# Kernel optimization log

Hardware: AMD Instinct MI355X
Metric: run time of the kernel (lower is better)

Reference implementation:

```python
import jax, jax.numpy as jnp
import numpy as np

N = 50000        # num nodes
F = 64           # feature_size
G = 64           # graph_embedding_size
C = 4            # num_edge_cat
NNZ = 800000     # edges per category
L0 = 128         # first MLP hidden layer
EMB = 64         # embedding_size
EPS = 1e-5


def _glorot(key, shape):
    fan_in, fan_out = shape[-2], shape[-1]
    lim = jnp.sqrt(6.0 / (fan_in + fan_out))
    return jax.random.uniform(key, shape, jnp.float32, -lim, lim)


def setup_inputs() -> dict:
    key = jax.random.key(0)
    ks = jax.random.split(key, 8)
    A = jax.random.randint(ks[0], (C, 2, NNZ), 0, N, dtype=jnp.int64)
    X = jax.random.normal(ks[1], (N, F), jnp.float32)
    Ws = _glorot(ks[2], (C, F, G))            # per-edge-cat projection
    W0 = _glorot(ks[3], (C * G, L0))          # Linear0 weight (in,out)
    b0 = jnp.zeros((L0,), jnp.float32)
    gamma = jnp.ones((L0,), jnp.float32)      # BatchNorm1d weight
    beta = jnp.zeros((L0,), jnp.float32)      # BatchNorm1d bias
    W1 = _glorot(ks[4], (L0, EMB))            # Linear1 weight (in,out)
    b1 = jnp.zeros((EMB,), jnp.float32)
    return {"A": A, "X": X, "Ws": Ws, "W0": W0, "b0": b0,
            "gamma": gamma, "beta": beta, "W1": W1, "b1": b1,
            "mini_batch": 0}


def reference(A, X, Ws, W0, b0, gamma, beta, W1, b1, mini_batch):
    # mini_batch == False path. Instead of materializing dense NxN adjacency,
    # aggregate directly over edge lists (same math: (E @ X)[i] = sum_{(i,j) in E} X[j]).
    n = X.shape[0]
    XW = jnp.einsum('nf,cfg->cng', X, Ws)                       # [C,N,G]
    def agg(edges, xw):                                          # edges [2,nnz], xw [N,G]
        return jax.ops.segment_sum(xw[edges[1]], edges[0], num_segments=n)
    H = jax.vmap(agg)(A, XW)                                     # [C,N,G]
    H = jnp.transpose(H, (1, 0, 2)).reshape(n, -1)               # concat over edge cats -> [N, C*G]
    # NodeEmbedding: Linear -> BatchNorm1d (training stats) -> ELU -> Linear
    h = H @ W0 + b0
    mean = jnp.mean(h, axis=0)
    var = jnp.mean((h - mean) ** 2, axis=0)                      # biased var, as torch BN
    h = (h - mean) * jax.lax.rsqrt(var + EPS) * gamma + beta
    h = jax.nn.elu(h)
    return h @ W1 + b1                                           # [N, EMB]
```

## Files before the change

### kernel.cpp

```cpp
#include <hip/hip_runtime.h>
#include <hip/hip_bf16.h>

#define NN    50000
#define CC    4
#define NNZV  800000
#define TOTE  (CC * NNZV)
#define NWG   1024
#define EPW   (TOTE / NWG)
#define NBKT  256
#define RCAP  18432
#define CAPB  26624
#define NRB   782
#define NXB   782

using bf16 = __hip_bfloat16;
typedef short short8 __attribute__((ext_vector_type(8)));
typedef float f32x4  __attribute__((ext_vector_type(4)));
typedef unsigned short u16x8 __attribute__((ext_vector_type(8)));

__device__ __forceinline__ float bfu2f(unsigned short u) {
    union { unsigned int i; float f; } v;
    v.i = ((unsigned int)u) << 16;
    return v.f;
}
__device__ __forceinline__ float cvt(float x) { return x; }
__device__ __forceinline__ float cvt(bf16 x)  { return __bfloat162float(x); }
__device__ __forceinline__ unsigned short tobits(float x) {
    bf16 t = __float2bfloat16(x);
    return *(unsigned short*)&t;
}

__device__ __forceinline__ void detect_flags(const unsigned int* __restrict__ Xw,
                                             const unsigned int* __restrict__ Aw,
                                             int* dcnt, int& f32f, int& i64f) {
    const int t = threadIdx.x, nthr = blockDim.x;
    if (t < 2) dcnt[t] = 0;
    __syncthreads();
    int c1 = 0;
    for (int i = t; i < 1024; i += nthr) {
        unsigned b = (Xw[i] >> 7) & 0xFF;
        if (b >= 118 && b <= 134) c1++;
    }
    if (c1) atomicAdd(&dcnt[0], c1);
    if (t < 128) { if (Aw[2 * t + 1] == 0) atomicAdd(&dcnt[1], 1); }
    __syncthreads();
    f32f = (dcnt[0] < 512) ? 1 : 0;
    i64f = (dcnt[1] >= 96) ? 1 : 0;
    __syncthreads();
}

template<typename TF>
__device__ __forceinline__ void pack_body(const TF* __restrict__ W0, const TF* __restrict__ W1,
                                          const TF* __restrict__ Ws, const TF* __restrict__ b0,
                                          const TF* __restrict__ b1,
                                          unsigned short* __restrict__ Wb,
                                          unsigned short* __restrict__ Wb1,
                                          float* __restrict__ bias0, float* __restrict__ bias1,
                                          int trip) {
    const int lane = trip & 63;
    const int q = lane >> 4, cI = lane & 15;
    if (trip < 4096) {
        const int k0 = trip >> 9, t8 = (trip >> 6) & 7;
        const int kbase = k0 * 32 + q * 8;
        const int col   = t8 * 16 + cI;
        const int c     = kbase >> 6;
        float w0c[64];
        #pragma unroll
        for (int g = 0; g < 64; ++g)
            w0c[g] = cvt(W0[(size_t)(c * 64 + g) * 128 + col]);
        #pragma unroll
        for (int j = 0; j < 8; ++j) {
            const int f = (kbase + j) & 63;
            const TF* wsrow = Ws + ((size_t)c * 64 + f) * 64;
            float acc = 0.f;
            #pragma unroll
            for (int g = 0; g < 64; ++g)
                acc += cvt(wsrow[g]) * w0c[g];
            Wb[(size_t)trip * 8 + j] = tobits(acc);
        }
    } else if (trip < 5120) {
        const int u = trip - 4096;
        const int k0 = u >> 8, t4 = (u >> 6) & 3;
        #pragma unroll
        for (int j = 0; j < 8; ++j)
            Wb1[(size_t)u * 8 + j] =
                tobits(cvt(W1[(size_t)(k0 * 32 + q * 8 + j) * 64 + t4 * 16 + cI]));
    } else if (trip < 5248) {
        bias0[trip - 5120] = cvt(b0[trip - 5120]);
    } else if (trip < 5312) {
        bias1[trip - 5248] = cvt(b1[trip - 5248]);
    }
}

__global__ __launch_bounds__(256) void pack_kernel(const void* X, const void* A,
                                                   const void* W0, const void* W1,
                                                   const void* Ws, const void* b0,
                                                   const void* b1,
                                                   unsigned short* Wb, unsigned short* Wb1,
                                                   float* bias0, float* bias1,
                                                   unsigned int* zero512) {
    __shared__ int dcnt[2];
    int f32f, i64f;
    detect_flags((const unsigned int*)X, (const unsigned int*)A, dcnt, f32f, i64f);
    const int t = threadIdx.x;
    if (blockIdx.x == 0) { zero512[t] = 0u; zero512[t + 256] = 0u; }
    const int trip = blockIdx.x * 256 + t;
    if (trip >= 5312) return;
    if (f32f) pack_body<float>((const float*)W0, (const float*)W1, (const float*)Ws,
                               (const float*)b0, (const float*)b1, Wb, Wb1, bias0, bias1, trip);
    else      pack_body<bf16> ((const bf16*)W0, (const bf16*)W1, (const bf16*)Ws,
                               (const bf16*)b0, (const bf16*)b1, Wb, Wb1, bias0, bias1, trip);
}

template<typename TI>
__device__ __forceinline__ void cscat2_body(const TI* __restrict__ A,
                                            unsigned int* __restrict__ gcur,
                                            unsigned int* __restrict__ recs,
                                            unsigned int* lh, unsigned int* lrec) {
    const int w = blockIdx.x, t = threadIdx.x;
    lh[t] = 0;
    __syncthreads();
    const int base = w * EPW;
    for (int i = t; i < EPW; i += 256) {
        const int e  = base + i;
        const int c  = e / NNZV;
        const int ei = e - c * NNZV;
        const int dst = (int)A[(size_t)(c * 2 + 0) * NNZV + ei];
        const int src = (int)A[(size_t)(c * 2 + 1) * NNZV + ei];
        unsigned int rec = 0xFFFFFFFFu;
        if ((unsigned)dst < NN && (unsigned)src < NN) {
            rec = ((unsigned)dst << 16) | (unsigned)src;
            atomicAdd(&lh[dst >> 8], 1u);
        }
        lrec[i] = rec;
    }
    __syncthreads();
    const unsigned int myslice = atomicAdd(&gcur[t], lh[t]);
    __syncthreads();
    lh[t] = myslice;
    __syncthreads();
    for (int i = t; i < EPW; i += 256) {
        const unsigned int rec = lrec[i];
        if (rec == 0xFFFFFFFFu) continue;
        const int e   = base + i;
        const int c   = e / NNZV;
        const int dst = (int)(rec >> 16);
        const int src = (int)(rec & 0xFFFFu);
        const int b   = dst >> 8;
        const unsigned int pos = atomicAdd(&lh[b], 1u);
        if (pos < RCAP)
            recs[(size_t)b * RCAP + pos] =
                ((unsigned)(dst & 255) << 18) | ((unsigned)c << 16) | (unsigned)src;
    }
}

__device__ __forceinline__ void xconv_body(const void* __restrict__ X, int f32f,
                                           unsigned short* __restrict__ Xb, int bidx) {
    const size_t base = (size_t)bidx * 4096 + (size_t)threadIdx.x * 16;
    #pragma unroll
    for (int i = 0; i < 4; ++i) {
        const size_t off = base + (size_t)i * 4;
        if (off < (size_t)NN * 64) {
            ushort4 o;
            if (f32f) {
                const float4 v = *(const float4*)((const float*)X + off);
                o.x = tobits(v.x); o.y = tobits(v.y); o.z = tobits(v.z); o.w = tobits(v.w);
            } else {
                o = *(const ushort4*)((const unsigned short*)X + off);
            }
            *(ushort4*)(Xb + off) = o;
        } else if (off < (size_t)(NN + 1) * 64) {
            *(ushort4*)(Xb + off) = make_ushort4(0, 0, 0, 0);
        }
    }
}

__global__ __launch_bounds__(256) void fused_kernel(const void* __restrict__ X,
                                                    const void* __restrict__ A,
                                                    unsigned short* __restrict__ Xb,
                                                    unsigned int* __restrict__ gcur,
                                                    unsigned int* __restrict__ recs) {
    __shared__ unsigned int Su[256 + EPW];
    __shared__ int dcnt[2];
    int f32f, i64f;
    detect_flags((const unsigned int*)X, (const unsigned int*)A, dcnt, f32f, i64f);
    if (blockIdx.x < NWG) {
        unsigned int* lh   = Su;
        unsigned int* lrec = Su + 256;
        if (i64f) cscat2_body<long long>((const long long*)A, gcur, recs, lh, lrec);
        else      cscat2_body<int>      ((const int*)A,       gcur, recs, lh, lrec);
    } else {
        xconv_body(X, f32f, Xb, blockIdx.x - NWG);
    }
}

__global__ __launch_bounds__(1024) void dfinal_kernel(const unsigned int* __restrict__ gcur,
                                                      const unsigned int* __restrict__ recs,
                                                      unsigned short* __restrict__ edge_src,
                                                      int2* __restrict__ segd) {
    __shared__ unsigned int lrec[RCAP];
    __shared__ unsigned int scnt[1024], soff[1024], send[1024];
    __shared__ unsigned int ts[256];
    const int b = blockIdx.x, t = threadIdx.x;
    const size_t obase = (size_t)b * CAPB;
    int n = (int)gcur[b];
    if (n > RCAP) n = RCAP;
    const size_t rbase = (size_t)b * RCAP;
    scnt[t] = 0;
    __syncthreads();
    for (int i = t; i < n; i += 1024) {
        const unsigned int r = recs[rbase + i];
        lrec[i] = r;
        const int seg = (int)(((r >> 18) & 255u) * 4u + ((r >> 16) & 3u));
        atomicAdd(&scnt[seg], 1u);
    }
    __syncthreads();
    unsigned int v0 = 0, v1 = 0, v2 = 0, v3 = 0;
    unsigned int p0 = 0, p1 = 0, p2 = 0, p3 = 0, s = 0;
    if (t < 256) {
        const int j0 = t * 4;
        v0 = scnt[j0]; v1 = scnt[j0 + 1]; v2 = scnt[j0 + 2]; v3 = scnt[j0 + 3];
        p0 = (v0 + 7u) & ~7u; p1 = (v1 + 7u) & ~7u;
        p2 = (v2 + 7u) & ~7u; p3 = (v3 + 7u) & ~7u;
        s = p0 + p1 + p2 + p3;
        ts[t] = s;
    }
    __syncthreads();
    for (int off = 1; off < 256; off <<= 1) {
        unsigned int val = 0;
        if (t < 256 && t >= off) val = ts[t - off];
        __syncthreads();
        if (t < 256) ts[t] += val;
        __syncthreads();
    }
    if (t < 256) {
        const int j0 = t * 4;
        unsigned int ex = ts[t] - s;
        soff[j0]     = ex;
        send[j0]     = ex + p0;
        soff[j0 + 1] = ex + p0;
        send[j0 + 1] = ex + p0 + p1;
        soff[j0 + 2] = ex + p0 + p1;
        send[j0 + 2] = ex + p0 + p1 + p2;
        soff[j0 + 3] = ex + p0 + p1 + p2;
        send[j0 + 3] = ex + s;
    }
    __syncthreads();
    {
        const int dst = b * 256 + (t >> 2);
        if (dst < NN) {
            int2 o; o.x = (int)(obase + soff[t]); o.y = (int)scnt[t];
            segd[b * 1024 + t] = o;
        }
    }
    __syncthreads();
    for (int i = t; i < n; i += 1024) {
        const unsigned int r = lrec[i];
        const int seg = (int)(((r >> 18) & 255u) * 4u + ((r >> 16) & 3u));
        const unsigned int pos = atomicAdd(&soff[seg], 1u);
        edge_src[obase + pos] = (unsigned short)(r & 0xFFFFu);
    }
    __syncthreads();
    {
        unsigned int j = soff[t];
        const unsigned int e = send[t];
        for (; j < e; ++j) edge_src[obase + j] = (unsigned short)NN;
    }
}

__global__ __launch_bounds__(256) void gather_kernel(const unsigned short* __restrict__ edge_src,
                                                     const int2* __restrict__ segd,
                                                     const unsigned short* __restrict__ Xb,
                                                     unsigned short* __restrict__ S) {
    const int t   = threadIdx.x;
    const int gid = t >> 4;
    const int li  = t & 15;
    const int g4  = li * 4;
    const int dst = blockIdx.x * 4 + (gid >> 2);
    const int c   = gid & 3;
    const int2 sd = segd[dst * 4 + c];
    const int cnt  = sd.y;
    const int pcnt = (cnt + 7) & ~7;
    const unsigned short* ep = edge_src + sd.x;
    f32x4 acc = (f32x4){0.f, 0.f, 0.f, 0.f};
    if (pcnt > 0) {
        u16x8 idx = *(const u16x8*)(ep);
        for (int e0 = 0; e0 < pcnt; e0 += 8) {
            const u16x8 nidx = *(const u16x8*)(ep + e0 + 8);
            ushort4 v0 = *(const ushort4*)(Xb + (size_t)idx[0] * 64 + g4);
            ushort4 v1 = *(const ushort4*)(Xb + (size_t)idx[1] * 64 + g4);
            ushort4 v2 = *(const ushort4*)(Xb + (size_t)idx[2] * 64 + g4);
            ushort4 v3 = *(const ushort4*)(Xb + (size_t)idx[3] * 64 + g4);
            ushort4 v4 = *(const ushort4*)(Xb + (size_t)idx[4] * 64 + g4);
            ushort4 v5 = *(const ushort4*)(Xb + (size_t)idx[5] * 64 + g4);
            ushort4 v6 = *(const ushort4*)(Xb + (size_t)idx[6] * 64 + g4);
            ushort4 v7 = *(const ushort4*)(Xb + (size_t)idx[7] * 64 + g4);
            acc[0] += bfu2f(v0.x); acc[1] += bfu2f(v0.y); acc[2] += bfu2f(v0.z); acc[3] += bfu2f(v0.w);
            acc[0] += bfu2f(v1.x); acc[1] += bfu2f(v1.y); acc[2] += bfu2f(v1.z); acc[3] += bfu2f(v1.w);
            acc[0] += bfu2f(v2.x); acc[1] += bfu2f(v2.y); acc[2] += bfu2f(v2.z); acc[3] += bfu2f(v2.w);
            acc[0] += bfu2f(v3.x); acc[1] += bfu2f(v3.y); acc[2] += bfu2f(v3.z); acc[3] += bfu2f(v3.w);
            acc[0] += bfu2f(v4.x); acc[1] += bfu2f(v4.y); acc[2] += bfu2f(v4.z); acc[3] += bfu2f(v4.w);
            acc[0] += bfu2f(v5.x); acc[1] += bfu2f(v5.y); acc[2] += bfu2f(v5.z); acc[3] += bfu2f(v5.w);
            acc[0] += bfu2f(v6.x); acc[1] += bfu2f(v6.y); acc[2] += bfu2f(v6.z); acc[3] += bfu2f(v6.w);
            acc[0] += bfu2f(v7.x); acc[1] += bfu2f(v7.y); acc[2] += bfu2f(v7.z); acc[3] += bfu2f(v7.w);
            idx = nidx;
        }
    }
    ushort4 o;
    o.x = tobits(acc[0]); o.y = tobits(acc[1]); o.z = tobits(acc[2]); o.w = tobits(acc[3]);
    *(ushort4*)(S + (size_t)dst * 256 + c * 64 + g4) = o;
}

__global__ __launch_bounds__(256) void l0_mfma(const unsigned short* __restrict__ Hg,
                                               const unsigned short* __restrict__ Wb,
                                               const float* __restrict__ bias0,
                                               unsigned short* __restrict__ hO,
                                               float* __restrict__ stats) {
    __shared__ unsigned short Hs[64 * 264];
    __shared__ float psum[128], psq[128];
    const int t = threadIdx.x;
    const int n0 = blockIdx.x * 64;
    #pragma unroll
    for (int i = 0; i < 16; ++i) {
        const int r = (t >> 6) + i * 4;
        const int k = (t & 63) * 4;
        const int row = n0 + r;
        ushort4 v = make_ushort4(0, 0, 0, 0);
        if (row < NN) v = *(const ushort4*)(Hg + (size_t)row * 256 + k);
        *(ushort4*)(&Hs[r * 264 + k]) = v;
    }
    if (t < 128) { psum[t] = 0.f; psq[t] = 0.f; }
    __syncthreads();
    const int w = t >> 6, lane = t & 63;
    const int q = lane >> 4, cI = lane & 15;
    f32x4 acc[8];
    #pragma unroll
    for (int i = 0; i < 8; ++i) acc[i] = (f32x4){0.f, 0.f, 0.f, 0.f};
    const unsigned short* arow = &Hs[(w * 16 + cI) * 264 + q * 8];
    #pragma unroll
    for (int k0 = 0; k0 < 8; ++k0) {
        short8 a = *(const short8*)(arow + k0 * 32);
        #pragma unroll
        for (int t8 = 0; t8 < 8; ++t8) {
            short8 b = *(const short8*)(Wb + ((size_t)(k0 * 8 + t8) * 64 + lane) * 8);
            acc[t8] = __builtin_amdgcn_mfma_f32_16x16x32_bf16(a, b, acc[t8], 0, 0, 0);
        }
    }
    __syncthreads();
    const int rloc  = w * 16 + q * 4;
    const int rbase = n0 + rloc;
    #pragma unroll
    for (int t8 = 0; t8 < 8; ++t8) {
        const int col = t8 * 16 + cI;
        const float bc = bias0[col];
        float s = 0.f, qq = 0.f;
        #pragma unroll
        for (int r = 0; r < 4; ++r) {
            float v = acc[t8][r] + bc;
            Hs[(rloc + r) * 136 + col] = tobits(v);
            if (rbase + r >= NN) v = 0.f;
            s += v; qq += v * v;
        }
        s  += __shfl_xor(s, 16, 64);  s  += __shfl_xor(s, 32, 64);
        qq += __shfl_xor(qq, 16, 64); qq += __shfl_xor(qq, 32, 64);
        if (q == 0) { atomicAdd(&psum[col], s); atomicAdd(&psq[col], qq); }
    }
    __syncthreads();
    if (t < 128) { atomicAdd(&stats[t], psum[t]); atomicAdd(&stats[128 + t], psq[t]); }
    #pragma unroll
    for (int i = 0; i < 4; ++i) {
        const int m    = t + i * 256;
        const int row  = m >> 4;
        const int col0 = (m & 15) * 8;
        const int grow = n0 + row;
        if (grow < NN) {
            *(ushort4*)(hO + (size_t)grow * 128 + col0)     = *(ushort4*)(&Hs[row * 136 + col0]);
            *(ushort4*)(hO + (size_t)grow * 128 + col0 + 4) = *(ushort4*)(&Hs[row * 136 + col0 + 4]);
        }
    }
}

__global__ __launch_bounds__(256) void l1_mfma(const void* __restrict__ X,
                                               const void* __restrict__ A,
                                               const unsigned short* __restrict__ hg,
                                               const float* __restrict__ stats,
                                               const void* __restrict__ gamma,
                                               const void* __restrict__ beta,
                                               const unsigned short* __restrict__ Wb1,
                                               const float* __restrict__ bias1,
                                               void* __restrict__ outv) {
    __shared__ unsigned short Es[64 * 136];
    __shared__ float coefL[256];
    __shared__ int dcnt[2];
    int f32f, i64f;
    detect_flags((const unsigned int*)X, (const unsigned int*)A, dcnt, f32f, i64f);
    const int t = threadIdx.x;
    if (t < 128) {
        const float invN = 1.0f / (float)NN;
        const float mean = stats[t] * invN;
        const float var  = stats[128 + t] * invN - mean * mean;
        const float inv  = rsqrtf(var + 1e-5f);
        const float ga = f32f ? ((const float*)gamma)[t] : cvt(((const bf16*)gamma)[t]);
        const float be = f32f ? ((const float*)beta)[t]  : cvt(((const bf16*)beta)[t]);
        const float a = ga * inv;
        coefL[t] = a;
        coefL[128 + t] = be - mean * a;
    }
    __syncthreads();
    const int n0 = blockIdx.x * 64;
    #pragma unroll
    for (int i = 0; i < 8; ++i) {
        const int r = (t >> 5) + i * 8;
        const int k = (t & 31) * 4;
        const int row = n0 + r;
        ushort4 o = make_ushort4(0, 0, 0, 0);
        if (row < NN) {
            ushort4 v = *(const ushort4*)(hg + (size_t)row * 128 + k);
            float f0 = coefL[k + 0] * bfu2f(v.x) + coefL[128 + k + 0];
            float f1 = coefL[k + 1] * bfu2f(v.y) + coefL[128 + k + 1];
            float f2 = coefL[k + 2] * bfu2f(v.z) + coefL[128 + k + 2];
            float f3 = coefL[k + 3] * bfu2f(v.w) + coefL[128 + k + 3];
            f0 = f0 > 0.f ? f0 : expm1f(f0);
            f1 = f1 > 0.f ? f1 : expm1f(f1);
            f2 = f2 > 0.f ? f2 : expm1f(f2);
            f3 = f3 > 0.f ? f3 : expm1f(f3);
            o.x = tobits(f0); o.y = tobits(f1); o.z = tobits(f2); o.w = tobits(f3);
        }
        *(ushort4*)(&Es[r * 136 + k]) = o;
    }
    __syncthreads();
    const int w = t >> 6, lane = t & 63;
    const int q = lane >> 4, cI = lane & 15;
    f32x4 acc[4];
    #pragma unroll
    for (int i = 0; i < 4; ++i) acc[i] = (f32x4){0.f, 0.f, 0.f, 0.f};
    const unsigned short* arow = &Es[(w * 16 + cI) * 136 + q * 8];
    #pragma unroll
    for (int k0 = 0; k0 < 4; ++k0) {
        short8 a = *(const short8*)(arow + k0 * 32);
        #pragma unroll
        for (int t4 = 0; t4 < 4; ++t4) {
            short8 b = *(const short8*)(Wb1 + ((size_t)(k0 * 4 + t4) * 64 + lane) * 8);
            acc[t4] = __builtin_amdgcn_mfma_f32_16x16x32_bf16(a, b, acc[t4], 0, 0, 0);
        }
    }
    __syncthreads();
    float* ot = (float*)Es;
    const int rloc = w * 16 + q * 4;
    #pragma unroll
    for (int t4 = 0; t4 < 4; ++t4) {
        const int col = t4 * 16 + cI;
        const float bc = bias1[col];
        #pragma unroll
        for (int r = 0; r < 4; ++r)
            ot[(rloc + r) * 68 + col] = acc[t4][r] + bc;
    }
    __syncthreads();
    #pragma unroll
    for (int i = 0; i < 4; ++i) {
        const int m    = t + i * 256;
        const int row  = m >> 4;
        const int col0 = (m & 15) * 4;
        const int grow = n0 + row;
        if (grow >= NN) continue;
        const float f0 = ot[row * 68 + col0 + 0];
        const float f1 = ot[row * 68 + col0 + 1];
        const float f2 = ot[row * 68 + col0 + 2];
        const float f3 = ot[row * 68 + col0 + 3];
        if (f32f) {
            float4 o; o.x = f0; o.y = f1; o.z = f2; o.w = f3;
            *(float4*)((float*)outv + (size_t)grow * 64 + col0) = o;
        } else {
            ushort4 o;
            o.x = tobits(f0); o.y = tobits(f1); o.z = tobits(f2); o.w = tobits(f3);
            *(ushort4*)((unsigned short*)outv + (size_t)grow * 64 + col0) = o;
        }
    }
}

extern "C" void kernel_launch(void* const* d_in, const int* in_sizes, int n_in,
                              void* d_out, int out_size, void* d_ws, size_t ws_size,
                              hipStream_t stream) {
    const void* A     = d_in[0];
    const void* X     = d_in[1];
    const void* Ws    = d_in[2];
    const void* W0    = d_in[3];
    const void* b0    = d_in[4];
    const void* gamma = d_in[5];
    const void* beta  = d_in[6];
    const void* W1    = d_in[7];
    const void* b1    = d_in[8];

    char* ws = (char*)d_ws;
    unsigned short* Xb       = (unsigned short*)(ws);
    unsigned short* S        = (unsigned short*)(ws + 6400256);
    unsigned short* h        = (unsigned short*)(ws + 32000256);
    unsigned int*   recs     = (unsigned int*)  (ws + 44800256);
    int2*           segd     = (int2*)          (ws + 59250944);
    unsigned short* edge_src = (unsigned short*)(ws + 60850944);
    float*          stats    = (float*)         (ws + 71287552);
    unsigned int*   gcur     = (unsigned int*)  (ws + 71288576);
    unsigned short* Wb       = (unsigned short*)(ws + 71289600);
    unsigned short* Wb1      = (unsigned short*)(ws + 71355136);
    float*          bias0    = (float*)         (ws + 71371520);
    float*          bias1    = (float*)         (ws + 71372032);

    pack_kernel  <<<21, 256, 0, stream>>>(X, A, W0, W1, Ws, b0, b1,
                                          Wb, Wb1, bias0, bias1,
                                          (unsigned int*)stats );
    fused_kernel <<<NWG + NXB, 256, 0, stream>>>(X, A, Xb, gcur, recs);
    dfinal_kernel<<<196, 1024, 0, stream>>>(gcur, recs, edge_src, segd);
    gather_kernel<<<12500, 256, 0, stream>>>(edge_src, segd, Xb, S);
    l0_mfma      <<<NRB, 256, 0, stream>>>(S, Wb, bias0, h, stats);
    l1_mfma      <<<NRB, 256, 0, stream>>>(X, A, h, stats, gamma, beta, Wb1, bias1, d_out);
}
```

Baseline: 258.8 us.

## Fuse destination sort and gather into one kernel with finer 64-node buckets

Edges are now bucketed into 64-node destination buckets, split across 8 partitions to spread global atomics, instead of 256-node buckets. The separate finalize and gather kernels are merged into one kernel per bucket that sorts edges into a shared-memory list and immediately gathers and sums X rows. This removes the global edge_src/segd round trip and one launch. In exchange it adds per-partition capacity limits (768 records per partition per bucket) that could overflow and drop edges on skewed inputs, and it launches far fewer gather blocks, which may lower latency hiding.

```diff
diff --git a/kernel.cpp b/kernel.cpp
--- a/kernel.cpp
+++ b/kernel.cpp
@@ -7,9 +7,10 @@
 #define TOTE  (CC * NNZV)
 #define NWG   1024
 #define EPW   (TOTE / NWG)
-#define NBKT  256
-#define RCAP  18432
-#define CAPB  26624
+#define NFB   782
+#define NPART 8
+#define RCAPV 768
+#define BCAP  (NPART * RCAPV)
 #define NRB   782
 #define NXB   782
 
@@ -98,12 +99,14 @@
                                                    const void* b1,
                                                    unsigned short* Wb, unsigned short* Wb1,
                                                    float* bias0, float* bias1,
-                                                   unsigned int* zero512) {
+                                                   unsigned int* zeroReg) {
     __shared__ int dcnt[2];
     int f32f, i64f;
     detect_flags((const unsigned int*)X, (const unsigned int*)A, dcnt, f32f, i64f);
     const int t = threadIdx.x;
-    if (blockIdx.x == 0) { zero512[t] = 0u; zero512[t + 256] = 0u; }
+    if (blockIdx.x == 0) {
+        for (int i = t; i < 8448; i += 256) zeroReg[i] = 0u;
+    }
     const int trip = blockIdx.x * 256 + t;
     if (trip >= 5312) return;
     if (f32f) pack_body<float>((const float*)W0, (const float*)W1, (const float*)Ws,
@@ -118,39 +121,46 @@
                                             unsigned int* __restrict__ recs,
                                             unsigned int* lh, unsigned int* lrec) {
     const int w = blockIdx.x, t = threadIdx.x;
-    lh[t] = 0;
-    __syncthreads();
-    const int base = w * EPW;
+    const int v = w & (NPART - 1);
+    #pragma unroll
+    for (int u = 0; u < 4; ++u) lh[t + u * 256] = 0;
+    __syncthreads();
+    const int base   = w * EPW;
+    const int c      = base / NNZV;
+    const int eibase = base - c * NNZV;
+    const TI* Ad = A + (size_t)(c * 2 + 0) * NNZV + eibase;
+    const TI* As = A + (size_t)(c * 2 + 1) * NNZV + eibase;
     for (int i = t; i < EPW; i += 256) {
-        const int e  = base + i;
-        const int c  = e / NNZV;
-        const int ei = e - c * NNZV;
-        const int dst = (int)A[(size_t)(c * 2 + 0) * NNZV + ei];
-        const int src = (int)A[(size_t)(c * 2 + 1) * NNZV + ei];
+        const int dst = (int)Ad[i];
+        const int src = (int)As[i];
         unsigned int rec = 0xFFFFFFFFu;
         if ((unsigned)dst < NN && (unsigned)src < NN) {
             rec = ((unsigned)dst << 16) | (unsigned)src;
-            atomicAdd(&lh[dst >> 8], 1u);
+            atomicAdd(&lh[dst >> 6], 1u);
         }
         lrec[i] = rec;
     }
     __syncthreads();
-    const unsigned int myslice = atomicAdd(&gcur[t], lh[t]);
-    __syncthreads();
-    lh[t] = myslice;
-    __syncthreads();
+    unsigned int cl[4], sl[4];
+    #pragma unroll
+    for (int u = 0; u < 4; ++u) cl[u] = lh[t + u * 256];
+    __syncthreads();
+    #pragma unroll
+    for (int u = 0; u < 4; ++u)
+        sl[u] = cl[u] ? atomicAdd(&gcur[(v << 10) + t + u * 256], cl[u]) : 0u;
+    #pragma unroll
+    for (int u = 0; u < 4; ++u) lh[t + u * 256] = sl[u];
+    __syncthreads();
+    const unsigned int cb = (unsigned)c << 16;
     for (int i = t; i < EPW; i += 256) {
         const unsigned int rec = lrec[i];
         if (rec == 0xFFFFFFFFu) continue;
-        const int e   = base + i;
-        const int c   = e / NNZV;
         const int dst = (int)(rec >> 16);
-        const int src = (int)(rec & 0xFFFFu);
-        const int b   = dst >> 8;
+        const int b   = dst >> 6;
         const unsigned int pos = atomicAdd(&lh[b], 1u);
-        if (pos < RCAP)
-            recs[(size_t)b * RCAP + pos] =
-                ((unsigned)(dst & 255) << 18) | ((unsigned)c << 16) | (unsigned)src;
+        if (pos < RCAPV)
+            recs[((size_t)b * NPART + v) * RCAPV + pos] =
+                ((unsigned)(dst & 63) << 18) | cb | (rec & 0xFFFFu);
     }
 }
 
@@ -180,13 +190,13 @@
                                                     unsigned short* __restrict__ Xb,
                                                     unsigned int* __restrict__ gcur,
                                                     unsigned int* __restrict__ recs) {
-    __shared__ unsigned int Su[256 + EPW];
+    __shared__ unsigned int Su[1024 + EPW];
     __shared__ int dcnt[2];
     int f32f, i64f;
     detect_flags((const unsigned int*)X, (const unsigned int*)A, dcnt, f32f, i64f);
     if (blockIdx.x < NWG) {
         unsigned int* lh   = Su;
-        unsigned int* lrec = Su + 256;
+        unsigned int* lrec = Su + 1024;
         if (i64f) cscat2_body<long long>((const long long*)A, gcur, recs, lh, lrec);
         else      cscat2_body<int>      ((const int*)A,       gcur, recs, lh, lrec);
     } else {
@@ -194,37 +204,30 @@
     }
 }
 
-__global__ __launch_bounds__(1024) void dfinal_kernel(const unsigned int* __restrict__ gcur,
+__global__ __launch_bounds__(512) void dgather_kernel(const unsigned int* __restrict__ gcur,
                                                       const unsigned int* __restrict__ recs,
-                                                      unsigned short* __restrict__ edge_src,
-                                                      int2* __restrict__ segd) {
-    __shared__ unsigned int lrec[RCAP];
-    __shared__ unsigned int scnt[1024], soff[1024], send[1024];
-    __shared__ unsigned int ts[256];
+                                                      const unsigned short* __restrict__ Xb,
+                                                      unsigned short* __restrict__ S) {
+    __shared__ unsigned short elist[8192];
+    __shared__ unsigned int scnt[256], sstart[256], scur[256], send[256], ts[256];
+    __shared__ unsigned int cntv[NPART];
     const int b = blockIdx.x, t = threadIdx.x;
-    const size_t obase = (size_t)b * CAPB;
-    int n = (int)gcur[b];
-    if (n > RCAP) n = RCAP;
-    const size_t rbase = (size_t)b * RCAP;
-    scnt[t] = 0;
-    __syncthreads();
-    for (int i = t; i < n; i += 1024) {
-        const unsigned int r = recs[rbase + i];
-        lrec[i] = r;
-        const int seg = (int)(((r >> 18) & 255u) * 4u + ((r >> 16) & 3u));
-        atomicAdd(&scnt[seg], 1u);
-    }
-    __syncthreads();
-    unsigned int v0 = 0, v1 = 0, v2 = 0, v3 = 0;
-    unsigned int p0 = 0, p1 = 0, p2 = 0, p3 = 0, s = 0;
-    if (t < 256) {
-        const int j0 = t * 4;
-        v0 = scnt[j0]; v1 = scnt[j0 + 1]; v2 = scnt[j0 + 2]; v3 = scnt[j0 + 3];
-        p0 = (v0 + 7u) & ~7u; p1 = (v1 + 7u) & ~7u;
-        p2 = (v2 + 7u) & ~7u; p3 = (v3 + 7u) & ~7u;
-        s = p0 + p1 + p2 + p3;
-        ts[t] = s;
-    }
+    if (t < NPART) {
+        unsigned int n = gcur[(t << 10) + b];
+        cntv[t] = n < RCAPV ? n : RCAPV;
+    }
+    if (t < 256) scnt[t] = 0;
+    __syncthreads();
+    const size_t rb = (size_t)b * BCAP;
+    #pragma unroll
+    for (int v = 0; v < NPART; ++v) {
+        const int n = (int)cntv[v];
+        for (int i = t; i < n; i += 512)
+            atomicAdd(&scnt[recs[rb + v * RCAPV + i] >> 16], 1u);
+    }
+    __syncthreads();
+    unsigned int myp = 0;
+    if (t < 256) { myp = (scnt[t] + 7u) & ~7u; ts[t] = myp; }
     __syncthreads();
     for (int off = 1; off < 256; off <<= 1) {
         unsigned int val = 0;
@@ -234,81 +237,62 @@
         __syncthreads();
     }
     if (t < 256) {
-        const int j0 = t * 4;
-        unsigned int ex = ts[t] - s;
-        soff[j0]     = ex;
-        send[j0]     = ex + p0;
-        soff[j0 + 1] = ex + p0;
-        send[j0 + 1] = ex + p0 + p1;
-        soff[j0 + 2] = ex + p0 + p1;
-        send[j0 + 2] = ex + p0 + p1 + p2;
-        soff[j0 + 3] = ex + p0 + p1 + p2;
-        send[j0 + 3] = ex + s;
-    }
-    __syncthreads();
-    {
-        const int dst = b * 256 + (t >> 2);
+        const unsigned int ex = ts[t] - myp;
+        sstart[t] = ex; scur[t] = ex; send[t] = ex + myp;
+        for (unsigned int j = ex + scnt[t]; j < ex + myp; ++j)
+            elist[j] = (unsigned short)NN;
+    }
+    __syncthreads();
+    #pragma unroll
+    for (int v = 0; v < NPART; ++v) {
+        const int n = (int)cntv[v];
+        for (int i = t; i < n; i += 512) {
+            const unsigned int r = recs[rb + v * RCAPV + i];
+            const unsigned int pos = atomicAdd(&scur[r >> 16], 1u);
+            elist[pos] = (unsigned short)(r & 0xFFFFu);
+        }
+    }
+    __syncthreads();
+    const int g  = t >> 4;
+    const int li = t & 15;
+    const int g4 = li * 4;
+    #pragma unroll
+    for (int s8 = 0; s8 < 8; ++s8) {
+        const int seg = g * 8 + s8;
+        const int dst = b * 64 + (seg >> 2);
+        const int c   = seg & 3;
+        const int start = (int)sstart[seg];
+        const int pcnt  = (int)(send[seg] - sstart[seg]);
+        f32x4 acc = (f32x4){0.f, 0.f, 0.f, 0.f};
+        if (pcnt > 0) {
+            u16x8 idx = *(const u16x8*)(elist + start);
+            for (int e0 = 0; e0 < pcnt; e0 += 8) {
+                const u16x8 nidx = *(const u16x8*)(elist + start + e0 + 8);
+                ushort4 v0 = *(const ushort4*)(Xb + (size_t)idx[0] * 64 + g4);
+                ushort4 v1 = *(const ushort4*)(Xb + (size_t)idx[1] * 64 + g4);
+                ushort4 v2 = *(const ushort4*)(Xb + (size_t)idx[2] * 64 + g4);
+                ushort4 v3 = *(const ushort4*)(Xb + (size_t)idx[3] * 64 + g4);
+                ushort4 v4 = *(const ushort4*)(Xb + (size_t)idx[4] * 64 + g4);
+                ushort4 v5 = *(const ushort4*)(Xb + (size_t)idx[5] * 64 + g4);
+                ushort4 v6 = *(const ushort4*)(Xb + (size_t)idx[6] * 64 + g4);
+                ushort4 v7 = *(const ushort4*)(Xb + (size_t)idx[7] * 64 + g4);
+                acc[0] += bfu2f(v0.x); acc[1] += bfu2f(v0.y); acc[2] += bfu2f(v0.z); acc[3] += bfu2f(v0.w);
+                acc[0] += bfu2f(v1.x); acc[1] += bfu2f(v1.y); acc[2] += bfu2f(v1.z); acc[3] += bfu2f(v1.w);
+                acc[0] += bfu2f(v2.x); acc[1] += bfu2f(v2.y); acc[2] += bfu2f(v2.z); acc[3] += bfu2f(v2.w);
+                acc[0] += bfu2f(v3.x); acc[1] += bfu2f(v3.y); acc[2] += bfu2f(v3.z); acc[3] += bfu2f(v3.w);
+                acc[0] += bfu2f(v4.x); acc[1] += bfu2f(v4.y); acc[2] += bfu2f(v4.z); acc[3] += bfu2f(v4.w);
+                acc[0] += bfu2f(v5.x); acc[1] += bfu2f(v5.y); acc[2] += bfu2f(v5.z); acc[3] += bfu2f(v5.w);
+                acc[0] += bfu2f(v6.x); acc[1] += bfu2f(v6.y); acc[2] += bfu2f(v6.z); acc[3] += bfu2f(v6.w);
+                acc[0] += bfu2f(v7.x); acc[1] += bfu2f(v7.y); acc[2] += bfu2f(v7.z); acc[3] += bfu2f(v7.w);
+                idx = nidx;
+            }
+        }
         if (dst < NN) {
-            int2 o; o.x = (int)(obase + soff[t]); o.y = (int)scnt[t];
-            segd[b * 1024 + t] = o;
-        }
-    }
-    __syncthreads();
-    for (int i = t; i < n; i += 1024) {
-        const unsigned int r = lrec[i];
-        const int seg = (int)(((r >> 18) & 255u) * 4u + ((r >> 16) & 3u));
-        const unsigned int pos = atomicAdd(&soff[seg], 1u);
-        edge_src[obase + pos] = (unsigned short)(r & 0xFFFFu);
-    }
-    __syncthreads();
-    {
-        unsigned int j = soff[t];
-        const unsigned int e = send[t];
-        for (; j < e; ++j) edge_src[obase + j] = (unsigned short)NN;
-    }
-}
-
-__global__ __launch_bounds__(256) void gather_kernel(const unsigned short* __restrict__ edge_src,
-                                                     const int2* __restrict__ segd,
-                                                     const unsigned short* __restrict__ Xb,
-                                                     unsigned short* __restrict__ S) {
-    const int t   = threadIdx.x;
-    const int gid = t >> 4;
-    const int li  = t & 15;
-    const int g4  = li * 4;
-    const int dst = blockIdx.x * 4 + (gid >> 2);
-    const int c   = gid & 3;
-    const int2 sd = segd[dst * 4 + c];
-    const int cnt  = sd.y;
-    const int pcnt = (cnt + 7) & ~7;
-    const unsigned short* ep = edge_src + sd.x;
-    f32x4 acc = (f32x4){0.f, 0.f, 0.f, 0.f};
-    if (pcnt > 0) {
-        u16x8 idx = *(const u16x8*)(ep);
-        for (int e0 = 0; e0 < pcnt; e0 += 8) {
-            const u16x8 nidx = *(const u16x8*)(ep + e0 + 8);
-            ushort4 v0 = *(const ushort4*)(Xb + (size_t)idx[0] * 64 + g4);
-            ushort4 v1 = *(const ushort4*)(Xb + (size_t)idx[1] * 64 + g4);
-            ushort4 v2 = *(const ushort4*)(Xb + (size_t)idx[2] * 64 + g4);
-            ushort4 v3 = *(const ushort4*)(Xb + (size_t)idx[3] * 64 + g4);
-            ushort4 v4 = *(const ushort4*)(Xb + (size_t)idx[4] * 64 + g4);
-            ushort4 v5 = *(const ushort4*)(Xb + (size_t)idx[5] * 64 + g4);
-            ushort4 v6 = *(const ushort4*)(Xb + (size_t)idx[6] * 64 + g4);
-            ushort4 v7 = *(const ushort4*)(Xb + (size_t)idx[7] * 64 + g4);
-            acc[0] += bfu2f(v0.x); acc[1] += bfu2f(v0.y); acc[2] += bfu2f(v0.z); acc[3] += bfu2f(v0.w);
-            acc[0] += bfu2f(v1.x); acc[1] += bfu2f(v1.y); acc[2] += bfu2f(v1.z); acc[3] += bfu2f(v1.w);
-            acc[0] += bfu2f(v2.x); acc[1] += bfu2f(v2.y); acc[2] += bfu2f(v2.z); acc[3] += bfu2f(v2.w);
-            acc[0] += bfu2f(v3.x); acc[1] += bfu2f(v3.y); acc[2] += bfu2f(v3.z); acc[3] += bfu2f(v3.w);
-            acc[0] += bfu2f(v4.x); acc[1] += bfu2f(v4.y); acc[2] += bfu2f(v4.z); acc[3] += bfu2f(v4.w);
-            acc[0] += bfu2f(v5.x); acc[1] += bfu2f(v5.y); acc[2] += bfu2f(v5.z); acc[3] += bfu2f(v5.w);
-            acc[0] += bfu2f(v6.x); acc[1] += bfu2f(v6.y); acc[2] += bfu2f(v6.z); acc[3] += bfu2f(v6.w);
-            acc[0] += bfu2f(v7.x); acc[1] += bfu2f(v7.y); acc[2] += bfu2f(v7.z); acc[3] += bfu2f(v7.w);
-            idx = nidx;
-        }
-    }
-    ushort4 o;
-    o.x = tobits(acc[0]); o.y = tobits(acc[1]); o.z = tobits(acc[2]); o.w = tobits(acc[3]);
-    *(ushort4*)(S + (size_t)dst * 256 + c * 64 + g4) = o;
+            ushort4 o;
+            o.x = tobits(acc[0]); o.y = tobits(acc[1]); o.z = tobits(acc[2]); o.w = tobits(acc[3]);
+            *(ushort4*)(S + (size_t)dst * 256 + c * 64 + g4) = o;
+        }
+    }
 }
 
 __global__ __launch_bounds__(256) void l0_mfma(const unsigned short* __restrict__ Hg,
@@ -496,21 +480,18 @@
     unsigned short* S        = (unsigned short*)(ws + 6400256);
     unsigned short* h        = (unsigned short*)(ws + 32000256);
     unsigned int*   recs     = (unsigned int*)  (ws + 44800256);
-    int2*           segd     = (int2*)          (ws + 59250944);
-    unsigned short* edge_src = (unsigned short*)(ws + 60850944);
-    float*          stats    = (float*)         (ws + 71287552);
-    unsigned int*   gcur     = (unsigned int*)  (ws + 71288576);
-    unsigned short* Wb       = (unsigned short*)(ws + 71289600);
-    unsigned short* Wb1      = (unsigned short*)(ws + 71355136);
-    float*          bias0    = (float*)         (ws + 71371520);
-    float*          bias1    = (float*)         (ws + 71372032);
-
-    pack_kernel  <<<21, 256, 0, stream>>>(X, A, W0, W1, Ws, b0, b1,
-                                          Wb, Wb1, bias0, bias1,
-                                          (unsigned int*)stats );
-    fused_kernel <<<NWG + NXB, 256, 0, stream>>>(X, A, Xb, gcur, recs);
-    dfinal_kernel<<<196, 1024, 0, stream>>>(gcur, recs, edge_src, segd);
-    gather_kernel<<<12500, 256, 0, stream>>>(edge_src, segd, Xb, S);
-    l0_mfma      <<<NRB, 256, 0, stream>>>(S, Wb, bias0, h, stats);
-    l1_mfma      <<<NRB, 256, 0, stream>>>(X, A, h, stats, gamma, beta, Wb1, bias1, d_out);
-}
+    float*          stats    = (float*)         (ws + 64018688);
+    unsigned int*   gcur     = (unsigned int*)  (ws + 64019712);
+    unsigned short* Wb       = (unsigned short*)(ws + 64052480);
+    unsigned short* Wb1      = (unsigned short*)(ws + 64118016);
+    float*          bias0    = (float*)         (ws + 64134400);
+    float*          bias1    = (float*)         (ws + 64134912);
+
+    pack_kernel   <<<21, 256, 0, stream>>>(X, A, W0, W1, Ws, b0, b1,
+                                           Wb, Wb1, bias0, bias1,
+                                           (unsigned int*)stats );
+    fused_kernel  <<<NWG + NXB, 256, 0, stream>>>(X, A, Xb, gcur, recs);
+    dgather_kernel<<<NFB, 512, 0, stream>>>(gcur, recs, Xb, S);
+    l0_mfma       <<<NRB, 256, 0, stream>>>(S, Wb, bias0, h, stats);
+    l1_mfma       <<<NRB, 256, 0, stream>>>(X, A, h, stats, gamma, beta, Wb1, bias1, d_out);
+}
```

Measured after the change: 236.3 us. 8.7% less time.
